# Kernel optimization log

Hardware: AMD Instinct MI355X
Metric: run time of the kernel (lower is better)

Reference implementation:

```python
import jax, jax.numpy as jnp
from jax import lax
import numpy as np

DIM = 256
HEADS = 8
DIM_HEAD = 32          # must equal W (see rearrange constraint in original code)
INNER = HEADS * DIM_HEAD
FF_INNER = DIM * 4
KH = 8                 # height_top_k (selects over dim_head axis due to axis mislabeling)
KW = 8                 # width_top_k  (selects over spatial H axis)
B, H, W = 8, 256, 32
EPS = 1e-5


def setup_inputs() -> dict:
    key = jax.random.key(0)
    ks = jax.random.split(key, 12)
    def rn(k, shape, fan_in):
        return jax.random.normal(k, shape, dtype=jnp.float32) / np.sqrt(fan_in)
    return {
        "x": jax.random.normal(ks[0], (B, DIM, H, W), dtype=jnp.float32),
        "cln_g": jnp.ones((1, DIM, 1, 1), dtype=jnp.float32),
        "cln_b": jnp.zeros((1, DIM, 1, 1), dtype=jnp.float32),
        "w_qkv": rn(ks[1], (INNER * 3, DIM), DIM),
        "w_out": rn(ks[2], (DIM, INNER), INNER),
        "b_out": jnp.zeros((DIM,), dtype=jnp.float32),
        "w_dw": rn(ks[3], (DIM, 1, 3, 3), 9),
        "b_dw": jnp.zeros((DIM,), dtype=jnp.float32),
        "w_comb": rn(ks[4], (DIM, DIM * 2), DIM * 2),
        "b_comb": jnp.zeros((DIM,), dtype=jnp.float32),
        "w_ff1": rn(ks[5], (FF_INNER, DIM), DIM),
        "b_ff1": jnp.zeros((FF_INNER,), dtype=jnp.float32),
        "w_ffdw": rn(ks[6], (FF_INNER, 1, 3, 3), 9),
        "b_ffdw": jnp.zeros((FF_INNER,), dtype=jnp.float32),
        "w_ff2": rn(ks[7], (DIM, FF_INNER), FF_INNER),
        "b_ff2": jnp.zeros((DIM,), dtype=jnp.float32),
    }


def _conv1x1(x, w, b=None):
    y = jnp.einsum('oc,bchw->bohw', w, x)
    return y if b is None else y + b[None, :, None, None]


def _dwconv3(x, w, b):
    y = lax.conv_general_dilated(x, w, (1, 1), 'SAME',
                                 feature_group_count=x.shape[1],
                                 dimension_numbers=('NCHW', 'OIHW', 'NCHW'))
    return y + b[None, :, None, None]


def _inorm(t):
    # nn.InstanceNorm2d(affine=False): normalize per (b, c) over spatial dims
    m = jnp.mean(t, axis=(2, 3), keepdims=True)
    v = jnp.var(t, axis=(2, 3), keepdims=True)
    return (t - m) / jnp.sqrt(v + EPS)


def _l2n(t):
    # F.normalize(dim=-1): here last axis is spatial W (acts as feature 'd')
    return t / jnp.clip(jnp.linalg.norm(t, axis=-1, keepdims=True), 1e-12)


def reference(x, cln_g, cln_b, w_qkv, w_out, b_out, w_dw, b_dw, w_comb, b_comb,
              w_ff1, b_ff1, w_ffdw, b_ffdw, w_ff2, b_ff2):
    b, c, h, w = x.shape
    # ---- DPSA branch ----
    mean = jnp.mean(x, axis=1, keepdims=True)
    var = jnp.var(x, axis=1, keepdims=True)
    xn = (x - mean) / jnp.sqrt(var + EPS) * cln_g + cln_b
    qkv = _conv1x1(xn, w_qkv)
    q, k, v = jnp.split(qkv, 3, axis=1)
    # '(b h) c x y' layout: axes are (b*heads, dim_head, H, W)
    q, k, v = (t.reshape(b * HEADS, DIM_HEAD, h, w) for t in (q, k, v))
    q, k = _l2n(q), _l2n(k)
    q_probe = q.sum(axis=(1, 2))                       # (bh, W)
    # 'height' selection -> actually over dim_head axis (axis 1)
    sh = jnp.einsum('bd,bhd->bh', q_probe, k.sum(axis=2))
    ih = lax.top_k(sh, KH)[1]                          # (bh, KH)
    k = jnp.take_along_axis(k, ih[:, :, None, None], axis=1)
    v = jnp.take_along_axis(v, ih[:, :, None, None], axis=1)
    # 'width' selection -> actually over spatial H axis (axis 2)
    sw = jnp.einsum('bd,bwd->bw', q_probe, k.sum(axis=1))
    iw = lax.top_k(sw, KW)[1]                          # (bh, KW)
    k = jnp.take_along_axis(k, iw[:, None, :, None], axis=2)
    v = jnp.take_along_axis(v, iw[:, None, :, None], axis=2)
    q2 = q.reshape(b * HEADS, DIM_HEAD * h, w)         # (bh, dh*H, W)
    k2 = k.reshape(b * HEADS, KH * KW, w)
    v2 = v.reshape(b * HEADS, KH * KW, w)
    attn = jax.nn.softmax(jnp.einsum('bid,bjd->bij', q2, k2), axis=-1)
    o = jnp.einsum('bij,bjd->bid', attn, v2)           # (bh, dh*H, W); dh == W
    # rearrange '(b h) (x y) d -> b (h d) x y'
    o = o.reshape(b, HEADS, h, w, w).transpose(0, 1, 4, 2, 3).reshape(b, HEADS * w, h, w)
    attn_branch = _conv1x1(o, w_out, b_out)
    # ---- conv branch + combine ----
    conv_branch = _dwconv3(x, w_dw, b_dw)
    comb = _conv1x1(jnp.concatenate([attn_branch, conv_branch], axis=1), w_comb, b_comb) + x
    # ---- feed-forward ----
    h1 = jax.nn.gelu(_inorm(_conv1x1(comb, w_ff1, b_ff1)), approximate=False)
    h2 = h1 + jax.nn.gelu(_inorm(_dwconv3(h1, w_ffdw, b_ffdw)), approximate=False)
    return _inorm(_conv1x1(h2, w_ff2, b_ff2))
```

## Files before the change

kernel.cpp:

```cpp
#include <hip/hip_runtime.h>
#include <hip/hip_fp16.h>
#include <math.h>

#define B_    8
#define CDIM  256
#define HH    256
#define WW    32
#define PP    8192
#define HEADS 8
#define FFI   1024

typedef _Float16 f16;
typedef _Float16 half8 __attribute__((ext_vector_type(8)));
typedef _Float16 half4 __attribute__((ext_vector_type(4)));
typedef _Float16 f16x2v __attribute__((ext_vector_type(2)));
typedef float f32x4 __attribute__((ext_vector_type(4)));

#define SOFT_BARRIER() asm volatile("s_waitcnt lgkmcnt(0)\n\ts_barrier" ::: "memory")

static const size_t OFF_QPROBE = 16908288;
static const size_t OFF_SH     = 16910336;
static const size_t OFF_IH     = 16912384;
static const size_t OFF_IW     = 16912896;
static const size_t OFF_STM    = 16913408;
static const size_t OFF_STR    = 16921600;
static const size_t OFF_VSEL   = 16929792;
static const size_t OFF_W16    = 17060864;

#define WH_QKV  0
#define WH_OUT  196608
#define WH_COMB 262144
#define WH_FF1  393216
#define WH_FF2  655360

__device__ __forceinline__ float gelu_f(float x) {
  float z = fabsf(x) * 0.70710678118f;
  float t = __builtin_amdgcn_rcpf(1.0f + 0.3275911f * z);
  float poly = t * (0.254829592f +
               t * (-0.284496736f +
               t * (1.421413741f +
               t * (-1.453152027f +
               t * 1.061405429f))));
  float e = 1.0f - poly * __expf(-z * z);
  return 0.5f * x * (1.0f + copysignf(e, x));
}

__global__ __launch_bounds__(256) void k_wcvt(const float* __restrict__ s0,
                                              const float* __restrict__ s1,
                                              const float* __restrict__ s2,
                                              const float* __restrict__ s3,
                                              const float* __restrict__ s4,
                                              f16* __restrict__ dst) {
  int blk = blockIdx.x;
  const float* src; size_t base;
  if (blk < 192)      { src = s0; base = WH_QKV;  }
  else if (blk < 256) { src = s1; base = WH_OUT;  blk -= 192; }
  else if (blk < 384) { src = s2; base = WH_COMB; blk -= 256; }
  else if (blk < 640) { src = s3; base = WH_FF1;  blk -= 384; }
  else                { src = s4; base = WH_FF2;  blk -= 640; }
  int off = blk * 1024 + threadIdx.x * 4;
  float4 v = *(const float4*)(src + off);
  half4 h; h[0] = (f16)v.x; h[1] = (f16)v.y; h[2] = (f16)v.z; h[3] = (f16)v.w;
  *(half4*)(dst + base + off) = h;
}

__global__ __launch_bounds__(256) void k_lnxn(const float* __restrict__ x,
                                              const float* __restrict__ g,
                                              const float* __restrict__ bb,
                                              f16* __restrict__ xn) {
  int idx = blockIdx.x * 256 + threadIdx.x;
  int b = idx >> 13, p = idx & 8191;
  const float* xp = x + (size_t)b * CDIM * PP + p;
  float s = 0.f, s2 = 0.f;
  for (int c = 0; c < CDIM; c++) { float v = xp[(size_t)c * PP]; s += v; s2 += v * v; }
  float m = s * (1.0f / CDIM);
  float var = s2 * (1.0f / CDIM) - m * m;
  float r = rsqrtf(var + 1e-5f);
  f16* xo = xn + (size_t)b * CDIM * PP + p;
  for (int c = 0; c < CDIM; c++)
    xo[(size_t)c * PP] = (f16)((xp[(size_t)c * PP] - m) * r * g[c] + bb[c]);
}

#define MF_STAGE                                                                   \
  int t = threadIdx.x;                                                             \
  int nw_ = gridDim.x * gridDim.y;                                                 \
  int hb_ = blockIdx.x + gridDim.x * blockIdx.y;                                   \
  int wk_ = (hb_ & 7) * (nw_ >> 3) + (hb_ >> 3);                                   \
  int gy_ = gridDim.y;                                                             \
  int sh_ = __ffs(gy_) - 1;                                                        \
  int p0 = (wk_ >> sh_) * 128, m0 = (wk_ & (gy_ - 1)) * 128, z = blockIdx.z;       \
  int lane = t & 63, wave = t >> 6;                                                \
  int wm = (wave >> 1) * 64, wp = (wave & 1) * 64;                                 \
  int col = lane & 15, quad = lane >> 4;                                           \
  f32x4 acc[4][4];                                                                 \
  _Pragma("unroll") for (int i = 0; i < 4; i++)                                    \
  _Pragma("unroll") for (int j = 0; j < 4; j++)                                    \
      acc[i][j] = (f32x4){0.f, 0.f, 0.f, 0.f};                                     \
  int am = t >> 1, ak = (t & 1) * 16;                                              \
  int bp = (t & 15) * 8, bk = (t >> 4) * 2;                                        \
  int erot = t & 7;                                                                \
  const f16* wr0 = W + (size_t)(m0 + am) * K + ak;                                 \
  const f16* br0 = inB + (size_t)bk * PP + p0 + bp;                                \
  half8 w0 = *(const half8*)wr0;                                                   \
  half8 w1 = *(const half8*)(wr0 + 8);                                             \
  half8 r0 = *(const half8*)br0;                                                   \
  half8 r1 = *(const half8*)(br0 + PP);                                            \
  for (int k0 = 0; k0 < K; k0 += 32) {                                             \
    *(half8*)&As[am][ak] = w0;                                                     \
    *(half8*)&As[am][ak + 8] = w1;                                                 \
    _Pragma("unroll") for (int e0 = 0; e0 < 8; e0++) {                             \
      int e = (e0 + erot) & 7;                                                     \
      f16x2v pr2; pr2[0] = r0[e]; pr2[1] = r1[e];                                  \
      *(f16x2v*)&Bs[bp + e][bk] = pr2;                                             \
    }                                                                              \
    SOFT_BARRIER();                                                                \
    int kn = (k0 + 32 < K) ? k0 + 32 : k0;                                         \
    w0 = *(const half8*)(wr0 + kn);                                                \
    w1 = *(const half8*)(wr0 + kn + 8);                                            \
    r0 = *(const half8*)(inB + (size_t)(kn + bk) * PP + p0 + bp);                  \
    r1 = *(const half8*)(inB + (size_t)(kn + bk + 1) * PP + p0 + bp);              \
    half8 af[4], bf[4];                                                            \
    _Pragma("unroll") for (int i = 0; i < 4; i++)                                  \
      af[i] = *(const half8*)&As[wm + i * 16 + col][quad * 8];                     \
    _Pragma("unroll") for (int j = 0; j < 4; j++)                                  \
      bf[j] = *(const half8*)&Bs[wp + j * 16 + col][quad * 8];                     \
    _Pragma("unroll") for (int i = 0; i < 4; i++)                                  \
    _Pragma("unroll") for (int j = 0; j < 4; j++)                                  \
        acc[i][j] = __builtin_amdgcn_mfma_f32_16x16x32_f16(af[i], bf[j],           \
                                                           acc[i][j], 0, 0, 0);    \
    SOFT_BARRIER();                                                                \
  }

__global__ __launch_bounds__(256) void k_mf(const f16* __restrict__ W,
                                            const f16* __restrict__ In, size_t inZ,
                                            f16* __restrict__ OutH,
                                            float* __restrict__ OutF, size_t outZ,
                                            const float* __restrict__ bias,
                                            const float* __restrict__ resid, size_t residZ,
                                            int K) {
  __shared__ f16 As[128][40];
  __shared__ f16 Bs[128][40];
  const f16* inB = In + (size_t)blockIdx.z * inZ;
  MF_STAGE
#pragma unroll
  for (int i = 0; i < 4; i++) {
    int mb = m0 + wm + i * 16 + quad * 4;
#pragma unroll
    for (int r = 0; r < 4; r++) {
      int m = mb + r;
      float bs = bias ? bias[m] : 0.f;
#pragma unroll
      for (int j = 0; j < 4; j++) {
        int p = p0 + wp + j * 16 + col;
        float v = acc[i][j][r] + bs;
        size_t off = (size_t)z * outZ + (size_t)m * PP + p;
        if (resid) v += resid[(size_t)z * residZ + (size_t)m * PP + p];
        if (OutF) __builtin_nontemporal_store(v, OutF + off);
        else __builtin_nontemporal_store((f16)v, OutH + off);
      }
    }
  }
}

#define MF_STAGE8                                                                  \
  int t = threadIdx.x;                                                             \
  int nw_ = gridDim.x * gridDim.y;                                                 \
  int hb_ = blockIdx.x + gridDim.x * blockIdx.y;                                   \
  int wk_ = (hb_ & 7) * (nw_ >> 3) + (hb_ >> 3);                                   \
  int gy_ = gridDim.y;                                                             \
  int sh_ = __ffs(gy_) - 1;                                                        \
  int p0 = (wk_ >> sh_) * 128, m0 = (wk_ & (gy_ - 1)) * 256, z = blockIdx.z;       \
  int lane = t & 63, wave = t >> 6;                                                \
  int wm = (wave >> 1) * 64, wp = (wave & 1) * 64;                                 \
  int col = lane & 15, quad = lane >> 4;                                           \
  f32x4 acc[4][4];                                                                 \
  _Pragma("unroll") for (int i = 0; i < 4; i++)                                    \
  _Pragma("unroll") for (int j = 0; j < 4; j++)                                    \
      acc[i][j] = (f32x4){0.f, 0.f, 0.f, 0.f};                                     \
  int am = t >> 1, ak = (t & 1) * 16;                                              \
  int bp = (t & 15) * 8, bk = (t >> 4) * 2;         \
  int erot = t & 7;                                                                \
  const f16* wr0 = W + (size_t)(m0 + am) * K + ak;                                 \
  const f16* br0 = inB + (size_t)(bk & 31) * PP + p0 + bp;                         \
  half8 w0 = *(const half8*)wr0;                                                   \
  half8 w1 = *(const half8*)(wr0 + 8);                                             \
  half8 r0 = {}, r1 = {};                                                          \
  if (t < 256) { r0 = *(const half8*)br0; r1 = *(const half8*)(br0 + PP); }        \
  for (int k0 = 0; k0 < K; k0 += 32) {                                             \
    *(half8*)&As[am][ak] = w0;                                                     \
    *(half8*)&As[am][ak + 8] = w1;                                                 \
    if (t < 256) {                                                                 \
      _Pragma("unroll") for (int e0 = 0; e0 < 8; e0++) {                           \
        int e = (e0 + erot) & 7;                                                   \
        f16x2v pr2; pr2[0] = r0[e]; pr2[1] = r1[e];                                \
        *(f16x2v*)&Bs[bp + e][bk] = pr2;                                           \
      }                                                                            \
    }                                                                              \
    SOFT_BARRIER();                                                                \
    int kn = (k0 + 32 < K) ? k0 + 32 : k0;                                         \
    w0 = *(const half8*)(wr0 + kn);                                                \
    w1 = *(const half8*)(wr0 + kn + 8);                                            \
    if (t < 256) {                                                                 \
      r0 = *(const half8*)(inB + (size_t)(kn + bk) * PP + p0 + bp);                \
      r1 = *(const half8*)(inB + (size_t)(kn + bk + 1) * PP + p0 + bp);            \
    }                                                                              \
    half8 af[4], bf[4];                                                            \
    _Pragma("unroll") for (int i = 0; i < 4; i++)                                  \
      af[i] = *(const half8*)&As[wm + i * 16 + col][quad * 8];                     \
    _Pragma("unroll") for (int j = 0; j < 4; j++)                                  \
      bf[j] = *(const half8*)&Bs[wp + j * 16 + col][quad * 8];                     \
    _Pragma("unroll") for (int i = 0; i < 4; i++)                                  \
    _Pragma("unroll") for (int j = 0; j < 4; j++)                                  \
        acc[i][j] = __builtin_amdgcn_mfma_f32_16x16x32_f16(af[i], bf[j],           \
                                                           acc[i][j], 0, 0, 0);    \
    SOFT_BARRIER();                                                                \
  }

__global__ __launch_bounds__(512) void k_mf8(const f16* __restrict__ W,
                                             const f16* __restrict__ In, size_t inZ,
                                             f16* __restrict__ OutH, size_t outZ,
                                             const float* __restrict__ bias,
                                             const float* __restrict__ resid, size_t residZ,
                                             int K) {
  __shared__ f16 As[256][40];
  __shared__ f16 Bs[128][40];
  const f16* inB = In + (size_t)blockIdx.z * inZ;
  MF_STAGE8
#pragma unroll
  for (int i = 0; i < 4; i++) {
    int mb = m0 + wm + i * 16 + quad * 4;
#pragma unroll
    for (int r = 0; r < 4; r++) {
      int m = mb + r;
      float bs = bias ? bias[m] : 0.f;
#pragma unroll
      for (int j = 0; j < 4; j++) {
        int p = p0 + wp + j * 16 + col;
        float v = acc[i][j][r] + bs;
        size_t off = (size_t)z * outZ + (size_t)m * PP + p;
        if (resid) v += resid[(size_t)z * residZ + (size_t)m * PP + p];
        __builtin_nontemporal_store((f16)v, OutH + off);
      }
    }
  }
}

__global__ __launch_bounds__(512) void k_mf_qk8(const f16* __restrict__ W,
                                                const f16* __restrict__ In, size_t inZ,
                                                f16* __restrict__ qkO, int K) {
  __shared__ f16 As[256][40];
  __shared__ f16 Bs[128][40];
  const f16* inB = In + (size_t)blockIdx.z * inZ;
  MF_STAGE8
#pragma unroll
  for (int i = 0; i < 4; i++) {
    int mb = m0 + wm + i * 16 + quad * 4;
#pragma unroll
    for (int r = 0; r < 4; r++) {
      int m = mb + r;
      size_t base = (size_t)z * 512 * PP + (size_t)m * PP;
#pragma unroll
      for (int jp = 0; jp < 2; jp++) {
        float a0 = acc[i][2 * jp][r], a1 = acc[i][2 * jp + 1][r];
        float ss = a0 * a0 + a1 * a1;
        ss += __shfl_xor(ss, 1);
        ss += __shfl_xor(ss, 2);
        ss += __shfl_xor(ss, 4);
        ss += __shfl_xor(ss, 8);
        float inv = 1.0f / fmaxf(sqrtf(ss), 1e-12f);
        int pa = p0 + wp + 2 * jp * 16 + col;
        __builtin_nontemporal_store((f16)(a0 * inv), qkO + base + pa);
        __builtin_nontemporal_store((f16)(a1 * inv), qkO + base + pa + 16);
      }
    }
  }
}

__global__ __launch_bounds__(256) void k_probe(const f16* __restrict__ qk,
                                               float* __restrict__ qprobe,
                                               float* __restrict__ sh) {
  __shared__ float red[64][32];
  __shared__ float qp[32];
  __shared__ float ksum[32][32];
  int bh = blockIdx.x, b = bh >> 3, hd = bh & 7;
  int t = threadIdx.x;
  const f16* qb = qk + ((size_t)(b * 512 + hd * 32)) * PP;
  {
    int g = t >> 2, wq = (t & 3) * 8;
    float s[8];
#pragma unroll
    for (int e = 0; e < 8; e++) s[e] = 0.f;
    for (int it = 0; it < 128; it++) {
      int row = g * 128 + it;
      half8 v = *(const half8*)(qb + (size_t)(row >> 8) * PP + (row & 255) * 32 + wq);
#pragma unroll
      for (int e = 0; e < 8; e++) s[e] += (float)v[e];
    }
#pragma unroll
    for (int e = 0; e < 8; e++) red[g][wq + e] = s[e];
  }
  __syncthreads();
  if (t < 32) {
    float a = 0.f;
    for (int g = 0; g < 64; g++) a += red[g][t];
    qp[t] = a;
    qprobe[bh * 32 + t] = a;
  }
  const f16* kb = qk + ((size_t)(b * 512 + 256 + hd * 32)) * PP;
  {
    int d = t >> 3, wq = (t & 7) * 4;
    float s[4] = {0.f, 0.f, 0.f, 0.f};
    for (int h = 0; h < 256; h++) {
      half4 v = *(const half4*)(kb + (size_t)d * PP + h * 32 + wq);
#pragma unroll
      for (int e = 0; e < 4; e++) s[e] += (float)v[e];
    }
#pragma unroll
    for (int e = 0; e < 4; e++) ksum[d][wq + e] = s[e];
  }
  __syncthreads();
  if (t < 32) {
    float a = 0.f;
    for (int w = 0; w < 32; w++) a += qp[w] * ksum[t][w];
    sh[bh * 32 + t] = a;
  }
}

__global__ __launch_bounds__(64) void k_topk_h(const float* __restrict__ sh, int* __restrict__ ih) {
  int bh = blockIdx.x;
  if (threadIdx.x != 0) return;
  float v[32];
#pragma unroll
  for (int i = 0; i < 32; i++) v[i] = sh[bh * 32 + i];
  for (int s = 0; s < 8; s++) {
    int bi = 0; float bv = v[0];
#pragma unroll
    for (int i = 1; i < 32; i++) { if (v[i] > bv) { bv = v[i]; bi = i; } }
    ih[bh * 8 + s] = bi;
    v[bi] = -3.4e38f;
  }
}

__global__ __launch_bounds__(256) void k_sw_topk(const f16* __restrict__ qk,
                                                 const float* __restrict__ qprobe,
                                                 const int* __restrict__ ih,
                                                 int* __restrict__ iw) {
  __shared__ float qp[32];
  __shared__ float sw[256];
  __shared__ int ihs[8];
  int bh = blockIdx.x, b = bh >> 3, hd = bh & 7;
  int t = threadIdx.x;
  if (t < 32) qp[t] = qprobe[bh * 32 + t];
  if (t < 8) ihs[t] = ih[bh * 8 + t];
  __syncthreads();
  const f16* kb = qk + ((size_t)(b * 512 + 256 + hd * 32)) * PP;
  float s = 0.f;
  for (int a = 0; a < 8; a++) {
    const f16* kd = kb + (size_t)ihs[a] * PP + t * 32;
#pragma unroll
    for (int w = 0; w < 32; w++) s += qp[w] * (float)kd[w];
  }
  sw[t] = s;
  __syncthreads();
  if (t == 0) {
    for (int sel = 0; sel < 8; sel++) {
      int bi = 0; float bv = sw[0];
      for (int i = 1; i < 256; i++) { if (sw[i] > bv) { bv = sw[i]; bi = i; } }
      iw[bh * 8 + sel] = bi;
      sw[bi] = -3.4e38f;
    }
  }
}

__global__ __launch_bounds__(256) void k_vsel2(const f16* __restrict__ xn,
                                               const f16* __restrict__ W16,
                                               const int* __restrict__ ih,
                                               const int* __restrict__ iw,
                                               float* __restrict__ vsel) {
  __shared__ f16 xg[64][264];
  __shared__ float wrow[8][64];
  __shared__ int ihs[8], iws8[8];
  int bh = blockIdx.x, b = bh >> 3, hd = bh & 7;
  int t = threadIdx.x;
  if (t < 8) { ihs[t] = ih[bh * 8 + t]; iws8[t] = iw[bh * 8 + t]; }
  __syncthreads();
  float acc[8];
#pragma unroll
  for (int a = 0; a < 8; a++) acc[a] = 0.f;
  for (int c0 = 0; c0 < 256; c0 += 64) {
    for (int rep = 0; rep < 2; rep++) {
      int cc = rep * 32 + (t >> 3);
      int seg = t & 7;
#pragma unroll
      for (int u = 0; u < 4; u++) {
        int h8 = seg * 4 + u;
        int bi = h8 >> 2, wq = (h8 & 3) * 8;
        half8 v = *(const half8*)(xn + ((size_t)(b * 256 + c0 + cc)) * PP + iws8[bi] * 32 + wq);
        *(half8*)&xg[cc][h8 * 8] = v;
      }
    }
    for (int rep = 0; rep < 2; rep++) {
      int idx = t + rep * 256;
      int a = idx >> 6, cc = idx & 63;
      wrow[a][cc] = (float)W16[(size_t)(512 + hd * 32 + ihs[a]) * 256 + c0 + cc];
    }
    __syncthreads();
    for (int cc = 0; cc < 64; cc++) {
      float xv = (float)xg[cc][t];
#pragma unroll
      for (int a = 0; a < 8; a++) acc[a] += wrow[a][cc] * xv;
    }
    __syncthreads();
  }
  int bi = t >> 5, w = t & 31;
#pragma unroll
  for (int a = 0; a < 8; a++)
    vsel[((size_t)bh * 64 + a * 8 + bi) * 32 + w] = acc[a];
}

__global__ __launch_bounds__(256) void k_attn_mf(const f16* __restrict__ qk,
                                                 const float* __restrict__ vsel,
                                                 const int* __restrict__ ih,
                                                 const int* __restrict__ iw,
                                                 f16* __restrict__ o_r) {
  __shared__ f16 Ks[64][40];
  __shared__ f16 Vt[32][72];
  __shared__ f16 Ps[4][32][72];
  __shared__ f16 Os[32][136];
  __shared__ int ihs[8], iws8[8];
  int bh = blockIdx.y, b = bh >> 3, hd = bh & 7;
  int t = threadIdx.x;
  if (t < 8) { ihs[t] = ih[bh * 8 + t]; iws8[t] = iw[bh * 8 + t]; }
  __syncthreads();
  {
    int j = t >> 2, wc = (t & 3) * 8;
    const f16* kb = qk + ((size_t)(b * 512 + 256 + hd * 32 + ihs[j >> 3])) * PP
                    + iws8[j & 7] * 32 + wc;
    *(half8*)&Ks[j][wc] = *(const half8*)kb;
  }
  for (int rep = 0; rep < 2; rep++) {
    int idx = t + rep * 256;
    int j = idx >> 3, w4 = (idx & 7) * 4;
    float4 v = *(const float4*)(vsel + ((size_t)bh * 64 + j) * 32 + w4);
    Vt[w4 + 0][j] = (f16)v.x; Vt[w4 + 1][j] = (f16)v.y;
    Vt[w4 + 2][j] = (f16)v.z; Vt[w4 + 3][j] = (f16)v.w;
  }
  __syncthreads();
  int wv = t >> 6, lane = t & 63, col = lane & 15, quad = lane >> 4;
  int i0 = blockIdx.x * 128;
  int dq = i0 >> 8;
  int hb = (i0 & 255) + wv * 32;
  const f16* qbase = qk + ((size_t)(b * 512 + hd * 32 + dq)) * PP;
  f32x4 sacc[2][4];
#pragma unroll
  for (int i = 0; i < 2; i++)
#pragma unroll
    for (int j = 0; j < 4; j++) sacc[i][j] = (f32x4){0.f, 0.f, 0.f, 0.f};
#pragma unroll
  for (int mt = 0; mt < 2; mt++) {
    half8 af = *(const half8*)(qbase + (size_t)(hb + mt * 16 + col) * 32 + quad * 8);
#pragma unroll
    for (int nt = 0; nt < 4; nt++) {
      half8 bf = *(const half8*)&Ks[nt * 16 + col][quad * 8];
      sacc[mt][nt] = __builtin_amdgcn_mfma_f32_16x16x32_f16(af, bf, sacc[mt][nt], 0, 0, 0);
    }
  }
#pragma unroll
  for (int mt = 0; mt < 2; mt++) {
#pragma unroll
    for (int r = 0; r < 4; r++) {
      float s0 = sacc[mt][0][r], s1 = sacc[mt][1][r], s2 = sacc[mt][2][r], s3 = sacc[mt][3][r];
      float mx = fmaxf(fmaxf(s0, s1), fmaxf(s2, s3));
      mx = fmaxf(mx, __shfl_xor(mx, 1));
      mx = fmaxf(mx, __shfl_xor(mx, 2));
      mx = fmaxf(mx, __shfl_xor(mx, 4));
      mx = fmaxf(mx, __shfl_xor(mx, 8));
      float e0 = __expf(s0 - mx), e1 = __expf(s1 - mx), e2 = __expf(s2 - mx), e3 = __expf(s3 - mx);
      float l = e0 + e1 + e2 + e3;
      l += __shfl_xor(l, 1);
      l += __shfl_xor(l, 2);
      l += __shfl_xor(l, 4);
      l += __shfl_xor(l, 8);
      float inv = 1.0f / l;
      int row = mt * 16 + quad * 4 + r;
      Ps[wv][row][0 * 16 + col] = (f16)(e0 * inv);
      Ps[wv][row][1 * 16 + col] = (f16)(e1 * inv);
      Ps[wv][row][2 * 16 + col] = (f16)(e2 * inv);
      Ps[wv][row][3 * 16 + col] = (f16)(e3 * inv);
    }
  }
  __syncthreads();
  f32x4 oacc[2][2];
#pragma unroll
  for (int i = 0; i < 2; i++)
#pragma unroll
    for (int j = 0; j < 2; j++) oacc[i][j] = (f32x4){0.f, 0.f, 0.f, 0.f};
#pragma unroll
  for (int kk = 0; kk < 2; kk++) {
    half8 ap[2], bv[2];
#pragma unroll
    for (int mt = 0; mt < 2; mt++) ap[mt] = *(const half8*)&Ps[wv][mt * 16 + col][kk * 32 + quad * 8];
#pragma unroll
    for (int wn = 0; wn < 2; wn++) bv[wn] = *(const half8*)&Vt[wn * 16 + col][kk * 32 + quad * 8];
#pragma unroll
    for (int mt = 0; mt < 2; mt++)
#pragma unroll
      for (int wn = 0; wn < 2; wn++)
        oacc[mt][wn] = __builtin_amdgcn_mfma_f32_16x16x32_f16(ap[mt], bv[wn], oacc[mt][wn], 0, 0, 0);
  }
#pragma unroll
  for (int mt = 0; mt < 2; mt++)
#pragma unroll
    for (int wn = 0; wn < 2; wn++)
#pragma unroll
      for (int r = 0; r < 4; r++)
        Os[wn * 16 + col][wv * 32 + mt * 16 + quad * 4 + r] = (f16)oacc[mt][wn][r];
  __syncthreads();
  {
    int dd = t >> 3, seg = t & 7;
#pragma unroll
    for (int u = 0; u < 2; u++) {
      int io = (seg * 2 + u) * 8;
      *(half8*)(o_r + ((size_t)(b * 256 + hd * 32 + dd)) * PP + i0 + io) = *(const half8*)&Os[dd][io];
    }
  }
}

__global__ __launch_bounds__(256) void k_dw(const float* __restrict__ in,
                                            const float* __restrict__ wdw,
                                            const float* __restrict__ bdw,
                                            f16* __restrict__ out) {
  int bc = blockIdx.x;
  int b = bc >> 8, c = bc & 255;
  int p = blockIdx.y * 256 + threadIdx.x;
  int x0 = p >> 5, y0 = p & 31;
  const float* ip = in + (size_t)bc * PP;
  const float* wp = wdw + c * 9;
  float s = bdw[c];
#pragma unroll
  for (int i = 0; i < 3; i++) {
    int xx = x0 + i - 1;
    if (xx < 0 || xx >= HH) continue;
#pragma unroll
    for (int j = 0; j < 3; j++) {
      int yy = y0 + j - 1;
      if (yy < 0 || yy >= WW) continue;
      s += wp[i * 3 + j] * ip[xx * 32 + yy];
    }
  }
  out[((size_t)(b * 512 + 256 + c)) * PP + p] = (f16)s;
}

__global__ __launch_bounds__(256) void k_ff_fused(const f16* __restrict__ h1,
                                                  const float* __restrict__ wdw,
                                                  const float* __restrict__ bdw,
                                                  f16* __restrict__ h2) {
  __shared__ float gbuf[256 * 33];
  __shared__ float redA[8], redB[8];
  int c = blockIdx.x, zz = blockIdx.y;
  int t = threadIdx.x;
  int wv = t >> 6, lane = t & 63;
  const f16* hp = h1 + ((size_t)zz * FFI + c) * PP;
  f16* out = h2 + ((size_t)zz * FFI + c) * PP;

  float v[32];
  float s = 0.f, s2 = 0.f;
#pragma unroll
  for (int u = 0; u < 4; u++) {
    half8 h = *(const half8*)(hp + (u * 256 + t) * 8);
#pragma unroll
    for (int e = 0; e < 8; e++) { float f = (float)h[e]; v[u * 8 + e] = f; s += f; s2 += f * f; }
  }
#pragma unroll
  for (int o = 32; o; o >>= 1) { s += __shfl_xor(s, o); s2 += __shfl_xor(s2, o); }
  if (lane == 0) { redA[wv] = s; redA[4 + wv] = s2; }
  __syncthreads();
  float m = (redA[0] + redA[1] + redA[2] + redA[3]) * (1.0f / PP);
  float s2a = (redA[4] + redA[5] + redA[6] + redA[7]) * (1.0f / PP);
  float r = rsqrtf(s2a - m * m + 1e-5f);

#pragma unroll
  for (int u = 0; u < 4; u++) {
    int base = (u * 256 + t) * 8;
    int row = base >> 5, colb = base & 31;
#pragma unroll
    for (int e = 0; e < 8; e++)
      gbuf[row * 33 + colb + e] = gelu_f((v[u * 8 + e] - m) * r);
  }
  __syncthreads();

  float wf[9];
#pragma unroll
  for (int i = 0; i < 9; i++) wf[i] = wdw[c * 9 + i];
  float bd = bdw[c];
  float g0[32];
#pragma unroll
  for (int y = 0; y < 32; y++) g0[y] = gbuf[t * 33 + y];
  const float* up = (t > 0) ? &gbuf[(t - 1) * 33] : nullptr;
  const float* dn = (t < 255) ? &gbuf[(t + 1) * 33] : nullptr;
  float d[32];
  float sd = 0.f, sd2 = 0.f;
#pragma unroll
  for (int y = 0; y < 32; y++) {
    float um1 = 0.f, u0 = 0.f, up1 = 0.f;
    float dm1 = 0.f, d0 = 0.f, dp1 = 0.f;
    if (up) { u0 = up[y]; if (y > 0) um1 = up[y - 1]; if (y < 31) up1 = up[y + 1]; }
    if (dn) { d0 = dn[y]; if (y > 0) dm1 = dn[y - 1]; if (y < 31) dp1 = dn[y + 1]; }
    float a = bd + wf[1] * u0 + wf[4] * g0[y] + wf[7] * d0;
    if (y > 0)  a += wf[0] * um1 + wf[3] * g0[y - 1] + wf[6] * dm1;
    if (y < 31) a += wf[2] * up1 + wf[5] * g0[y + 1] + wf[8] * dp1;
    d[y] = a; sd += a; sd2 += a * a;
  }
#pragma unroll
  for (int o = 32; o; o >>= 1) { sd += __shfl_xor(sd, o); sd2 += __shfl_xor(sd2, o); }
  if (lane == 0) { redB[wv] = sd; redB[4 + wv] = sd2; }
  __syncthreads();
  float dm = (redB[0] + redB[1] + redB[2] + redB[3]) * (1.0f / PP);
  float dv = (redB[4] + redB[5] + redB[6] + redB[7]) * (1.0f / PP);
  float dr = rsqrtf(dv - dm * dm + 1e-5f);

#pragma unroll
  for (int y = 0; y < 32; y++)
    gbuf[t * 33 + y] = g0[y] + gelu_f((d[y] - dm) * dr);
  __syncthreads();

#pragma unroll
  for (int u = 0; u < 4; u++) {
    int base = (u * 256 + t) * 8;
    int row = base >> 5, colb = base & 31;
    half8 h;
#pragma unroll
    for (int e = 0; e < 8; e++) h[e] = (f16)gbuf[row * 33 + colb + e];
    *(half8*)(out + base) = h;
  }
}

__global__ __launch_bounds__(256) void k_istats(const float* __restrict__ in,
                                                float* __restrict__ stm,
                                                float* __restrict__ str) {
  __shared__ float ss[256], ss2[256];
  int row = blockIdx.x, t = threadIdx.x;
  const float* p = in + (size_t)row * PP;
  float s = 0.f, s2 = 0.f;
  for (int i = t; i < PP; i += 256) { float v = p[i]; s += v; s2 += v * v; }
  ss[t] = s; ss2[t] = s2;
  __syncthreads();
  for (int off = 128; off; off >>= 1) {
    if (t < off) { ss[t] += ss[t + off]; ss2[t] += ss2[t + off]; }
    __syncthreads();
  }
  if (t == 0) {
    float m = ss[0] * (1.0f / PP);
    float var = ss2[0] * (1.0f / PP) - m * m;
    stm[row] = m;
    str[row] = rsqrtf(var + 1e-5f);
  }
}

__global__ __launch_bounds__(256) void k_napply(float* __restrict__ io,
                                                const float* __restrict__ stm,
                                                const float* __restrict__ str) {
  size_t idx = (size_t)blockIdx.x * 256 + threadIdx.x;
  int row = (int)(idx >> 13);
  io[idx] = (io[idx] - stm[row]) * str[row];
}

extern "C" void kernel_launch(void* const* d_in, const int* in_sizes, int n_in,
                              void* d_out, int out_size, void* d_ws, size_t ws_size,
                              hipStream_t stream) {
  const float* x      = (const float*)d_in[0];
  const float* cln_g  = (const float*)d_in[1];
  const float* cln_b  = (const float*)d_in[2];
  const float* w_qkv  = (const float*)d_in[3];
  const float* w_out  = (const float*)d_in[4];
  const float* b_out  = (const float*)d_in[5];
  const float* w_dw   = (const float*)d_in[6];
  const float* b_dw   = (const float*)d_in[7];
  const float* w_comb = (const float*)d_in[8];
  const float* b_comb = (const float*)d_in[9];
  const float* w_ff1  = (const float*)d_in[10];
  const float* b_ff1  = (const float*)d_in[11];
  const float* w_ffdw = (const float*)d_in[12];
  const float* b_ffdw = (const float*)d_in[13];
  const float* w_ff2  = (const float*)d_in[14];
  const float* b_ff2  = (const float*)d_in[15];
  float* outF = (float*)d_out;

  float* ws = (float*)d_ws;
  f16* qk    = (f16*)ws;
  f16* bv512 = (f16*)ws;
  f16* h1    = (f16*)ws;
  f16* xn    = (f16*)d_out;
  f16* o_r   = (f16*)d_out;
  f16* combT = (f16*)d_out;
  float* qprobe = ws + OFF_QPROBE;
  float* sh     = ws + OFF_SH;
  int*   ih     = (int*)(ws + OFF_IH);
  int*   iw     = (int*)(ws + OFF_IW);
  float* stm    = ws + OFF_STM;
  float* str    = ws + OFF_STR;
  float* vsel   = ws + OFF_VSEL;
  f16*   W16    = (f16*)(ws + OFF_W16);

  hipLaunchKernelGGL(k_wcvt, dim3(896), dim3(256), 0, stream,
                     w_qkv, w_out, w_comb, w_ff1, w_ff2, W16);
  hipLaunchKernelGGL(k_lnxn, dim3(256), dim3(256), 0, stream, x, cln_g, cln_b, xn);
  hipLaunchKernelGGL(k_mf_qk8, dim3(64, 2, 8), dim3(512), 0, stream,
                     W16 + WH_QKV, xn, (size_t)CDIM * PP, qk, 256);
  hipLaunchKernelGGL(k_probe, dim3(64), dim3(256), 0, stream, qk, qprobe, sh);
  hipLaunchKernelGGL(k_topk_h, dim3(64), dim3(64), 0, stream, sh, ih);
  hipLaunchKernelGGL(k_sw_topk, dim3(64), dim3(256), 0, stream, qk, qprobe, ih, iw);
  hipLaunchKernelGGL(k_vsel2, dim3(64), dim3(256), 0, stream, xn, W16 + WH_QKV, ih, iw, vsel);
  hipLaunchKernelGGL(k_attn_mf, dim3(64, 64), dim3(256), 0, stream, qk, vsel, ih, iw, o_r);
  hipLaunchKernelGGL(k_mf8, dim3(64, 1, 8), dim3(512), 0, stream,
                     W16 + WH_OUT, o_r, (size_t)CDIM * PP, bv512, (size_t)512 * PP,
                     b_out, (const float*)nullptr, (size_t)0, 256);
  hipLaunchKernelGGL(k_dw, dim3(2048, 32), dim3(256), 0, stream, x, w_dw, b_dw, bv512);
  hipLaunchKernelGGL(k_mf8, dim3(64, 1, 8), dim3(512), 0, stream,
                     W16 + WH_COMB, bv512, (size_t)512 * PP, combT, (size_t)CDIM * PP,
                     b_comb, x, (size_t)CDIM * PP, 512);
  for (int b = 4; b >= 0; b -= 4) {
    hipLaunchKernelGGL(k_mf8, dim3(64, 4, 4), dim3(512), 0, stream,
                       W16 + WH_FF1, combT + (size_t)b * CDIM * PP, (size_t)CDIM * PP,
                       h1, (size_t)FFI * PP, b_ff1,
                       (const float*)nullptr, (size_t)0, 256);
    hipLaunchKernelGGL(k_ff_fused, dim3(FFI, 4), dim3(256), 0, stream,
                       h1, w_ffdw, b_ffdw, h1);
    hipLaunchKernelGGL(k_mf, dim3(64, 2, 4), dim3(256), 0, stream,
                       W16 + WH_FF2, h1, (size_t)FFI * PP,
                       (f16*)nullptr, outF + (size_t)b * CDIM * PP, (size_t)CDIM * PP,
                       b_ff2, (const float*)nullptr, (size_t)0, 1024);
  }
  hipLaunchKernelGGL(k_istats, dim3(2048), dim3(256), 0, stream, outF, stm, str);
  hipLaunchKernelGGL(k_napply, dim3(65536), dim3(256), 0, stream, outF, stm, str);
}
```

Measured before the change: 969.4 us.

## Split probe reduction across 4096 blocks and fuse top-k; drop nontemporal stores

The single 64-block probe kernel, which serially summed q and k rows, becomes a 64x64-grid partial-sum kernel (one row per block) plus a small finalize kernel. The finalize kernel computes the q probe, the scores and the height top-k, folding in the old top-k kernel. This is meant to fix the low parallelism of the old reduction on a large GPU, at the cost of an extra partial buffer round trip. Separately, the GEMM epilogues switch from nontemporal stores to plain stores so outputs can stay in cache for the next consumer kernel.

```diff
diff --git a/kernel.cpp b/kernel.cpp
--- a/kernel.cpp
+++ b/kernel.cpp
@@ -18,6 +18,7 @@
 
 #define SOFT_BARRIER() asm volatile("s_waitcnt lgkmcnt(0)\n\ts_barrier" ::: "memory")
 
+static const size_t OFF_PPART  = 16777216;
 static const size_t OFF_QPROBE = 16908288;
 static const size_t OFF_SH     = 16910336;
 static const size_t OFF_IH     = 16912384;
@@ -155,8 +156,8 @@
         float v = acc[i][j][r] + bs;
         size_t off = (size_t)z * outZ + (size_t)m * PP + p;
         if (resid) v += resid[(size_t)z * residZ + (size_t)m * PP + p];
-        if (OutF) __builtin_nontemporal_store(v, OutF + off);
-        else __builtin_nontemporal_store((f16)v, OutH + off);
+        if (OutF) OutF[off] = v;
+        else OutH[off] = (f16)v;
       }
     }
   }
@@ -239,7 +240,7 @@
         float v = acc[i][j][r] + bs;
         size_t off = (size_t)z * outZ + (size_t)m * PP + p;
         if (resid) v += resid[(size_t)z * residZ + (size_t)m * PP + p];
-        __builtin_nontemporal_store((f16)v, OutH + off);
+        OutH[off] = (f16)v;
       }
     }
   }
@@ -269,75 +270,68 @@
         ss += __shfl_xor(ss, 8);
         float inv = 1.0f / fmaxf(sqrtf(ss), 1e-12f);
         int pa = p0 + wp + 2 * jp * 16 + col;
-        __builtin_nontemporal_store((f16)(a0 * inv), qkO + base + pa);
-        __builtin_nontemporal_store((f16)(a1 * inv), qkO + base + pa + 16);
+        qkO[base + pa] = (f16)(a0 * inv);
+        qkO[base + pa + 16] = (f16)(a1 * inv);
       }
     }
   }
 }
 
-__global__ __launch_bounds__(256) void k_probe(const f16* __restrict__ qk,
-                                               float* __restrict__ qprobe,
-                                               float* __restrict__ sh) {
+__global__ __launch_bounds__(256) void k_psum(const f16* __restrict__ qk,
+                                              float* __restrict__ part) {
   __shared__ float red[64][32];
-  __shared__ float qp[32];
-  __shared__ float ksum[32][32];
-  int bh = blockIdx.x, b = bh >> 3, hd = bh & 7;
+  int bh = blockIdx.x, y = blockIdx.y;
+  int b = bh >> 3, hd = bh & 7;
   int t = threadIdx.x;
-  const f16* qb = qk + ((size_t)(b * 512 + hd * 32)) * PP;
-  {
-    int g = t >> 2, wq = (t & 3) * 8;
-    float s[8];
-#pragma unroll
-    for (int e = 0; e < 8; e++) s[e] = 0.f;
-    for (int it = 0; it < 128; it++) {
-      int row = g * 128 + it;
-      half8 v = *(const half8*)(qb + (size_t)(row >> 8) * PP + (row & 255) * 32 + wq);
-#pragma unroll
-      for (int e = 0; e < 8; e++) s[e] += (float)v[e];
-    }
-#pragma unroll
-    for (int e = 0; e < 8; e++) red[g][wq + e] = s[e];
-  }
+  int row = (y < 32) ? (b * 512 + hd * 32 + y)
+                     : (b * 512 + 256 + hd * 32 + (y - 32));
+  const f16* rp = qk + (size_t)row * PP;
+  int g = t >> 2, w8 = (t & 3) * 8;
+  float s[8];
+#pragma unroll
+  for (int e = 0; e < 8; e++) s[e] = 0.f;
+  for (int h = g; h < 256; h += 64) {
+    half8 v = *(const half8*)(rp + h * 32 + w8);
+#pragma unroll
+    for (int e = 0; e < 8; e++) s[e] += (float)v[e];
+  }
+#pragma unroll
+  for (int e = 0; e < 8; e++) red[g][w8 + e] = s[e];
   __syncthreads();
   if (t < 32) {
     float a = 0.f;
-    for (int g = 0; g < 64; g++) a += red[g][t];
-    qp[t] = a;
-    qprobe[bh * 32 + t] = a;
-  }
-  const f16* kb = qk + ((size_t)(b * 512 + 256 + hd * 32)) * PP;
-  {
-    int d = t >> 3, wq = (t & 7) * 4;
-    float s[4] = {0.f, 0.f, 0.f, 0.f};
-    for (int h = 0; h < 256; h++) {
-      half4 v = *(const half4*)(kb + (size_t)d * PP + h * 32 + wq);
-#pragma unroll
-      for (int e = 0; e < 4; e++) s[e] += (float)v[e];
-    }
-#pragma unroll
-    for (int e = 0; e < 4; e++) ksum[d][wq + e] = s[e];
-  }
-  __syncthreads();
+    for (int gg = 0; gg < 64; gg++) a += red[gg][t];
+    part[((size_t)bh * 64 + y) * 32 + t] = a;
+  }
+}
+
+__global__ __launch_bounds__(64) void k_pfin(const float* __restrict__ part,
+                                             float* __restrict__ qprobe,
+                                             int* __restrict__ ih) {
+  __shared__ float qps[32], shs[32];
+  int bh = blockIdx.x, t = threadIdx.x;
+  const float* pb = part + (size_t)bh * 2048;
   if (t < 32) {
     float a = 0.f;
-    for (int w = 0; w < 32; w++) a += qp[w] * ksum[t][w];
-    sh[bh * 32 + t] = a;
-  }
-}
-
-__global__ __launch_bounds__(64) void k_topk_h(const float* __restrict__ sh, int* __restrict__ ih) {
-  int bh = blockIdx.x;
-  if (threadIdx.x != 0) return;
-  float v[32];
-#pragma unroll
-  for (int i = 0; i < 32; i++) v[i] = sh[bh * 32 + i];
-  for (int s = 0; s < 8; s++) {
-    int bi = 0; float bv = v[0];
-#pragma unroll
-    for (int i = 1; i < 32; i++) { if (v[i] > bv) { bv = v[i]; bi = i; } }
-    ih[bh * 8 + s] = bi;
-    v[bi] = -3.4e38f;
+    for (int d = 0; d < 32; d++) a += pb[d * 32 + t];
+    qps[t] = a;
+    qprobe[bh * 32 + t] = a;
+  }
+  __syncthreads();
+  if (t < 32) {
+    float a = 0.f;
+    const float* kp = pb + (size_t)(32 + t) * 32;
+    for (int w = 0; w < 32; w++) a += qps[w] * kp[w];
+    shs[t] = a;
+  }
+  __syncthreads();
+  if (t == 0) {
+    for (int s = 0; s < 8; s++) {
+      int bi = 0; float bv = shs[0];
+      for (int i = 1; i < 32; i++) { if (shs[i] > bv) { bv = shs[i]; bi = i; } }
+      ih[bh * 8 + s] = bi;
+      shs[bi] = -3.4e38f;
+    }
   }
 }
 
@@ -693,8 +687,8 @@
   f16* xn    = (f16*)d_out;
   f16* o_r   = (f16*)d_out;
   f16* combT = (f16*)d_out;
+  float* ppart  = ws + OFF_PPART;
   float* qprobe = ws + OFF_QPROBE;
-  float* sh     = ws + OFF_SH;
   int*   ih     = (int*)(ws + OFF_IH);
   int*   iw     = (int*)(ws + OFF_IW);
   float* stm    = ws + OFF_STM;
@@ -707,8 +701,8 @@
   hipLaunchKernelGGL(k_lnxn, dim3(256), dim3(256), 0, stream, x, cln_g, cln_b, xn);
   hipLaunchKernelGGL(k_mf_qk8, dim3(64, 2, 8), dim3(512), 0, stream,
                      W16 + WH_QKV, xn, (size_t)CDIM * PP, qk, 256);
-  hipLaunchKernelGGL(k_probe, dim3(64), dim3(256), 0, stream, qk, qprobe, sh);
-  hipLaunchKernelGGL(k_topk_h, dim3(64), dim3(64), 0, stream, sh, ih);
+  hipLaunchKernelGGL(k_psum, dim3(64, 64), dim3(256), 0, stream, qk, ppart);
+  hipLaunchKernelGGL(k_pfin, dim3(64), dim3(64), 0, stream, ppart, qprobe, ih);
   hipLaunchKernelGGL(k_sw_topk, dim3(64), dim3(256), 0, stream, qk, qprobe, ih, iw);
   hipLaunchKernelGGL(k_vsel2, dim3(64), dim3(256), 0, stream, xn, W16 + WH_QKV, ih, iw, vsel);
   hipLaunchKernelGGL(k_attn_mf, dim3(64, 64), dim3(256), 0, stream, qk, vsel, ih, iw, o_r);
```

After: 900.5 us. 1.08x faster.
